# Kernel optimization log

Measured on AMD Instinct MI355X. Metric: run time of the kernel, lower is better.

Reference implementation:

```python
import jax, jax.numpy as jnp
import numpy as np

B, L, H = 32, 2048, 768   # batch, BERT seq len, hidden size (fc is Linear(768,1))
D, C = 32, 64             # max doc len (clauses per doc), max clause len (tokens per clause)
NEG = -900000.0           # masked_fill value from the original module


def setup_inputs() -> dict:
    key = jax.random.key(0)
    k1, k2, k3, k4, k5 = jax.random.split(key, 5)
    return {
        "hidden_states": jax.random.normal(k1, (B, L, H), jnp.float32),
        "fc_w": jax.random.normal(k2, (H,), jnp.float32) * 0.02,
        "fc_b": jax.random.normal(k3, (1,), jnp.float32) * 0.02,
        "clause_len": jax.random.randint(k4, (B, D), 0, C),
        "doc_len": jax.random.randint(k5, (B,), 0, D),
    }


def reference(hidden_states, fc_w, fc_b, clause_len, doc_len):
    b, l, h = hidden_states.shape
    d = clause_len.shape[1]
    c = C
    # Exclusive prefix sum of clause lengths = start offset of each clause in the token stream.
    offsets = jnp.cumsum(clause_len, axis=1) - clause_len            # [B, D]
    pos = offsets[:, :, None] + jnp.arange(c)[None, None, :]         # [B, D, C] token index per slot
    # Valid-slot mask: within clause length AND within doc length (matches mask_all in torch code).
    mask = (jnp.arange(c)[None, None, :] < clause_len[:, :, None]) & \
           (jnp.arange(d)[None, :, None] < doc_len[:, None, None])   # [B, D, C] bool
    idx = jnp.clip(pos, 0, l - 1)
    # Ragged gather: pick tokens for every (doc, clause, slot), zero out padding slots.
    sent = jnp.take_along_axis(hidden_states, idx.reshape(b, -1)[:, :, None], axis=1)
    sent = sent.reshape(b, d, c, h) * mask[..., None].astype(hidden_states.dtype)  # [B, D, C, H]
    # fc(hidden).squeeze(-1), mask, softmax over tokens of each clause.
    alpha = jnp.einsum('bdch,h->bdc', sent, fc_w) + fc_b[0]          # [B, D, C]
    alpha = jnp.where(mask, alpha, NEG)
    w = jax.nn.softmax(alpha, axis=-1)                               # [B, D, C]
    # Attention-pooled clause representations.
    return jnp.einsum('bdc,bdch->bdh', w, sent)                      # [B, D, H]
```

## Files before the change

### kernel.cpp

```cpp
#include <hip/hip_runtime.h>
#include <hip/hip_bf16.h>

#define Bc 32
#define Lc 2048
#define Hc 768
#define Dc 32
#define Cc 64
#define WAVES 8
#define TPB (WAVES * 64)

__global__ __launch_bounds__(TPB, 4) void clause_attn_fused(
    const float* __restrict__ hs,
    const float* __restrict__ fc_w,
    const int*   __restrict__ clause_len,
    const int*   __restrict__ doc_len,
    float*       __restrict__ out)
{
    const int bd   = blockIdx.x;
    const int b    = bd >> 5;
    const int d    = bd & 31;
    const int tid  = threadIdx.x;
    const int lane = tid & 63;
    const int wave = tid >> 6;

    __shared__ float s_m[WAVES];
    __shared__ float s_s[WAVES];
    __shared__ float s_acc[WAVES][Hc];
    __shared__ int   s_n, s_off;

    if (wave == 0) {
        int v = (lane < Dc) ? clause_len[b * Dc + lane] : 0;
        int sum = v;
        #pragma unroll
        for (int s = 1; s < 32; s <<= 1) {
            int o = __shfl_up(sum, s, 64);
            if (lane >= s) sum += o;
        }
        if (lane == d) {
            s_off = sum - v;
            s_n   = (d < doc_len[b]) ? v : 0;
        }
    }
    __syncthreads();

    const int n   = s_n;
    const int off = s_off;
    float* ob = out + (size_t)bd * Hc;

    if (n == 0) {
        ob[tid] = 0.0f;
        if (tid < Hc - TPB) ob[TPB + tid] = 0.0f;
        return;
    }

    const int hbase = lane * 4;
    const float4 w0 = *(const float4*)(fc_w + hbase);
    const float4 w1 = *(const float4*)(fc_w + 256 + hbase);
    const float4 w2 = *(const float4*)(fc_w + 512 + hbase);

    const float* base = hs + (size_t)b * Lc * Hc;

    float m = -INFINITY, ssum = 0.0f;
    float4 a0 = {0,0,0,0}, a1 = {0,0,0,0}, a2 = {0,0,0,0};

    int c = wave;
    float4 v0, v1, v2;
    if (c < n) {
        const float* r = base + (size_t)(off + c) * Hc;
        v0 = *(const float4*)(r + hbase);
        v1 = *(const float4*)(r + 256 + hbase);
        v2 = *(const float4*)(r + 512 + hbase);
    }
    for (; c < n; c += WAVES) {
        float4 u0, u1, u2;
        const int cn = c + WAVES;
        if (cn < n) {
            const float* r = base + (size_t)(off + cn) * Hc;
            u0 = *(const float4*)(r + hbase);
            u1 = *(const float4*)(r + 256 + hbase);
            u2 = *(const float4*)(r + 512 + hbase);
        }
        float p = v0.x*w0.x + v0.y*w0.y + v0.z*w0.z + v0.w*w0.w
                + v1.x*w1.x + v1.y*w1.y + v1.z*w1.z + v1.w*w1.w
                + v2.x*w2.x + v2.y*w2.y + v2.z*w2.z + v2.w*w2.w;
        #pragma unroll
        for (int s = 32; s > 0; s >>= 1)
            p += __shfl_xor(p, s, 64);
        const float M     = fmaxf(m, p);
        const float scale = __expf(m - M);
        const float e     = __expf(p - M);
        ssum = ssum * scale + e;
        a0.x = a0.x*scale + e*v0.x;  a0.y = a0.y*scale + e*v0.y;
        a0.z = a0.z*scale + e*v0.z;  a0.w = a0.w*scale + e*v0.w;
        a1.x = a1.x*scale + e*v1.x;  a1.y = a1.y*scale + e*v1.y;
        a1.z = a1.z*scale + e*v1.z;  a1.w = a1.w*scale + e*v1.w;
        a2.x = a2.x*scale + e*v2.x;  a2.y = a2.y*scale + e*v2.y;
        a2.z = a2.z*scale + e*v2.z;  a2.w = a2.w*scale + e*v2.w;
        m = M;
        v0 = u0; v1 = u1; v2 = u2;
    }

    if (lane == 0) { s_m[wave] = m; s_s[wave] = ssum; }
    *(float4*)&s_acc[wave][hbase]       = a0;
    *(float4*)&s_acc[wave][256 + hbase] = a1;
    *(float4*)&s_acc[wave][512 + hbase] = a2;
    __syncthreads();

    float M = -INFINITY;
    #pragma unroll
    for (int w = 0; w < WAVES; ++w) M = fmaxf(M, s_m[w]);
    float f[WAVES];
    float S = 0.0f;
    #pragma unroll
    for (int w = 0; w < WAVES; ++w) {
        f[w] = __expf(s_m[w] - M);
        S += f[w] * s_s[w];
    }
    const float rinv = 1.0f / S;

    float r0 = 0.0f;
    #pragma unroll
    for (int w = 0; w < WAVES; ++w) r0 += f[w] * s_acc[w][tid];
    ob[tid] = r0 * rinv;
    if (tid < Hc - TPB) {
        float r1 = 0.0f;
        #pragma unroll
        for (int w = 0; w < WAVES; ++w) r1 += f[w] * s_acc[w][TPB + tid];
        ob[TPB + tid] = r1 * rinv;
    }
}

extern "C" void kernel_launch(void* const* d_in, const int* in_sizes, int n_in,
                              void* d_out, int out_size, void* d_ws, size_t ws_size,
                              hipStream_t stream) {
    const float* hs         = (const float*)d_in[0];
    const float* fc_w       = (const float*)d_in[1];
    const int*   clause_len = (const int*)d_in[3];
    const int*   doc_len    = (const int*)d_in[4];
    float*       out        = (float*)d_out;

    clause_attn_fused<<<Bc * Dc, TPB, 0, stream>>>(hs, fc_w, clause_len, doc_len, out);
}
```

Measured before the change: 19.23 us.

## Halve waves per block and deepen row prefetch with two rows per iteration

Cuts the block to 4 waves and has each wave process two clause rows per iteration, keeping two future row pairs in flight in registers (triple-buffered loads). The online softmax is updated once for both rows using fused multiply-adds. The goal is more memory-level parallelism per wave and a cheaper cross-wave merge with fewer waves. The cost is higher register pressure, and fewer waves per block for short clauses, which may reduce occupancy or leave the memory pipe under-filled.

```diff
diff --git a/kernel.cpp b/kernel.cpp
--- a/kernel.cpp
+++ b/kernel.cpp
@@ -6,7 +6,7 @@
 #define Hc 768
 #define Dc 32
 #define Cc 64
-#define WAVES 8
+#define WAVES 4
 #define TPB (WAVES * 64)
 
 __global__ __launch_bounds__(TPB, 4) void clause_attn_fused(
@@ -48,8 +48,7 @@
     float* ob = out + (size_t)bd * Hc;
 
     if (n == 0) {
-        ob[tid] = 0.0f;
-        if (tid < Hc - TPB) ob[TPB + tid] = 0.0f;
+        ob[tid] = 0.0f; ob[tid + 256] = 0.0f; ob[tid + 512] = 0.0f;
         return;
     }
 
@@ -59,46 +58,68 @@
     const float4 w2 = *(const float4*)(fc_w + 512 + hbase);
 
     const float* base = hs + (size_t)b * Lc * Hc;
+    const float4 z4 = {0.f, 0.f, 0.f, 0.f};
+
+    #define LOADROW(c, x0, x1, x2)                                      \
+        if ((c) < n) {                                                  \
+            const float* r_ = base + (size_t)(off + (c)) * Hc + hbase;  \
+            x0 = *(const float4*)(r_);                                  \
+            x1 = *(const float4*)(r_ + 256);                            \
+            x2 = *(const float4*)(r_ + 512);                            \
+        } else { x0 = z4; x1 = z4; x2 = z4; }
 
     float m = -INFINITY, ssum = 0.0f;
-    float4 a0 = {0,0,0,0}, a1 = {0,0,0,0}, a2 = {0,0,0,0};
+    float4 a0 = z4, a1 = z4, a2 = z4;
 
+    float4 A00, A01, A02, A10, A11, A12;
+    float4 B00, B01, B02, B10, B11, B12;
     int c = wave;
-    float4 v0, v1, v2;
-    if (c < n) {
-        const float* r = base + (size_t)(off + c) * Hc;
-        v0 = *(const float4*)(r + hbase);
-        v1 = *(const float4*)(r + 256 + hbase);
-        v2 = *(const float4*)(r + 512 + hbase);
+    LOADROW(c,     A00, A01, A02);
+    LOADROW(c + 4, A10, A11, A12);
+    LOADROW(c + 8,  B00, B01, B02);
+    LOADROW(c + 12, B10, B11, B12);
+
+    for (; c < n; c += 8) {
+        float4 C00, C01, C02, C10, C11, C12;
+        LOADROW(c + 16, C00, C01, C02);
+        LOADROW(c + 20, C10, C11, C12);
+
+        float p0 = A00.x*w0.x + A00.y*w0.y + A00.z*w0.z + A00.w*w0.w
+                 + A01.x*w1.x + A01.y*w1.y + A01.z*w1.z + A01.w*w1.w
+                 + A02.x*w2.x + A02.y*w2.y + A02.z*w2.z + A02.w*w2.w;
+        float p1 = A10.x*w0.x + A10.y*w0.y + A10.z*w0.z + A10.w*w0.w
+                 + A11.x*w1.x + A11.y*w1.y + A11.z*w1.z + A11.w*w1.w
+                 + A12.x*w2.x + A12.y*w2.y + A12.z*w2.z + A12.w*w2.w;
+        #pragma unroll
+        for (int s = 32; s > 0; s >>= 1) {
+            p0 += __shfl_xor(p0, s, 64);
+            p1 += __shfl_xor(p1, s, 64);
+        }
+        if (c + 4 >= n) p1 = -INFINITY;
+
+        const float M     = fmaxf(m, fmaxf(p0, p1));
+        const float scale = __expf(m - M);
+        const float e0    = __expf(p0 - M);
+        const float e1    = __expf(p1 - M);
+        ssum = ssum * scale + e0 + e1;
+        a0.x = fmaf(e1, A10.x, fmaf(e0, A00.x, a0.x * scale));
+        a0.y = fmaf(e1, A10.y, fmaf(e0, A00.y, a0.y * scale));
+        a0.z = fmaf(e1, A10.z, fmaf(e0, A00.z, a0.z * scale));
+        a0.w = fmaf(e1, A10.w, fmaf(e0, A00.w, a0.w * scale));
+        a1.x = fmaf(e1, A11.x, fmaf(e0, A01.x, a1.x * scale));
+        a1.y = fmaf(e1, A11.y, fmaf(e0, A01.y, a1.y * scale));
+        a1.z = fmaf(e1, A11.z, fmaf(e0, A01.z, a1.z * scale));
+        a1.w = fmaf(e1, A11.w, fmaf(e0, A01.w, a1.w * scale));
+        a2.x = fmaf(e1, A12.x, fmaf(e0, A02.x, a2.x * scale));
+        a2.y = fmaf(e1, A12.y, fmaf(e0, A02.y, a2.y * scale));
+        a2.z = fmaf(e1, A12.z, fmaf(e0, A02.z, a2.z * scale));
+        a2.w = fmaf(e1, A12.w, fmaf(e0, A02.w, a2.w * scale));
+        m = M;
+
+        A00 = B00; A01 = B01; A02 = B02; A10 = B10; A11 = B11; A12 = B12;
+        B00 = C00; B01 = C01; B02 = C02; B10 = C10; B11 = C11; B12 = C12;
     }
-    for (; c < n; c += WAVES) {
-        float4 u0, u1, u2;
-        const int cn = c + WAVES;
-        if (cn < n) {
-            const float* r = base + (size_t)(off + cn) * Hc;
-            u0 = *(const float4*)(r + hbase);
-            u1 = *(const float4*)(r + 256 + hbase);
-            u2 = *(const float4*)(r + 512 + hbase);
-        }
-        float p = v0.x*w0.x + v0.y*w0.y + v0.z*w0.z + v0.w*w0.w
-                + v1.x*w1.x + v1.y*w1.y + v1.z*w1.z + v1.w*w1.w
-                + v2.x*w2.x + v2.y*w2.y + v2.z*w2.z + v2.w*w2.w;
-        #pragma unroll
-        for (int s = 32; s > 0; s >>= 1)
-            p += __shfl_xor(p, s, 64);
-        const float M     = fmaxf(m, p);
-        const float scale = __expf(m - M);
-        const float e     = __expf(p - M);
-        ssum = ssum * scale + e;
-        a0.x = a0.x*scale + e*v0.x;  a0.y = a0.y*scale + e*v0.y;
-        a0.z = a0.z*scale + e*v0.z;  a0.w = a0.w*scale + e*v0.w;
-        a1.x = a1.x*scale + e*v1.x;  a1.y = a1.y*scale + e*v1.y;
-        a1.z = a1.z*scale + e*v1.z;  a1.w = a1.w*scale + e*v1.w;
-        a2.x = a2.x*scale + e*v2.x;  a2.y = a2.y*scale + e*v2.y;
-        a2.z = a2.z*scale + e*v2.z;  a2.w = a2.w*scale + e*v2.w;
-        m = M;
-        v0 = u0; v1 = u1; v2 = u2;
-    }
+    #undef LOADROW
 
     if (lane == 0) { s_m[wave] = m; s_s[wave] = ssum; }
     *(float4*)&s_acc[wave][hbase]       = a0;
@@ -118,15 +139,13 @@
     }
     const float rinv = 1.0f / S;
 
-    float r0 = 0.0f;
     #pragma unroll
-    for (int w = 0; w < WAVES; ++w) r0 += f[w] * s_acc[w][tid];
-    ob[tid] = r0 * rinv;
-    if (tid < Hc - TPB) {
-        float r1 = 0.0f;
+    for (int chunk = 0; chunk < 3; ++chunk) {
+        const int h = chunk * TPB + tid;
+        float r = 0.0f;
         #pragma unroll
-        for (int w = 0; w < WAVES; ++w) r1 += f[w] * s_acc[w][TPB + tid];
-        ob[TPB + tid] = r1 * rinv;
+        for (int w = 0; w < WAVES; ++w) r += f[w] * s_acc[w][h];
+        ob[h] = r * rinv;
     }
 }
 
```

Result: slower. 19.72 us (+2.6%).
